# Optimization experiments

Hardware: AMD Instinct MI355X
Metric: run time of the kernel (lower is better)

The kernel has to match this reference:

```python
import jax, jax.numpy as jnp
import numpy as np

N = 100000
IN_DIM = 256
OUT_DIM = 256
E = 3200000
SLOPE = 0.2


def setup_inputs() -> dict:
    key = jax.random.key(0)
    ks = jax.random.split(key, 14)
    xav = lambda k, shape: jax.random.normal(k, shape, jnp.float32) * np.sqrt(2.0 / sum(shape))
    inp = {
        "H": jax.random.normal(ks[0], (N, IN_DIM), jnp.float32),
        "W0": xav(ks[1], (IN_DIM, OUT_DIM)),
        "W1": xav(ks[2], (IN_DIM, OUT_DIM)),
        "W2": xav(ks[3], (IN_DIM, OUT_DIM)),
        "a0": xav(ks[4], (2 * OUT_DIM,)),
        "a1": xav(ks[5], (2 * OUT_DIM,)),
        "a2": xav(ks[6], (2 * OUT_DIM,)),
        "bias": jnp.zeros((OUT_DIM,), jnp.float32),
    }
    for i, r in enumerate(["0", "1", "2"]):
        inp["row" + r] = jax.random.randint(ks[7 + 2 * i], (E,), 0, N, jnp.int32)
        inp["col" + r] = jax.random.randint(ks[8 + 2 * i], (E,), 0, N, jnp.int32)
    return inp


def _gat_type(H, W, a, row, col):
    # Wh: [N, out_dim]
    Wh = H @ W
    # attention logits per edge: leaky_relu(a_dst . Wh[row] + a_src . Wh[col])
    s_dst = Wh @ a[:OUT_DIM]   # [N]
    s_src = Wh @ a[OUT_DIM:]   # [N]
    e = jax.nn.leaky_relu(s_dst[row] + s_src[col], SLOPE)  # [E]
    # segment softmax over destination node (row)
    e_max = jax.ops.segment_max(e, row, num_segments=N)    # [N]
    e_shifted = jnp.exp(e - e_max[row])
    e_sum = jax.ops.segment_sum(e_shifted, row, num_segments=N)
    alpha = e_shifted / jnp.maximum(e_sum[row], 1e-12)     # [E]
    # weighted aggregation of source features into destinations
    return jax.ops.segment_sum(alpha[:, None] * Wh[col], row, num_segments=N)


def reference(H, row0, col0, row1, col1, row2, col2, W0, W1, W2, a0, a1, a2, bias):
    out = _gat_type(H, W0, a0, row0, col0)
    out = out + _gat_type(H, W1, a1, row1, col1)
    out = out + _gat_type(H, W2, a2, row2, col2)
    return out + bias
```

## Files before the change

kernel.cpp:

```cpp
#include <hip/hip_runtime.h>
#include <cstdint>
#include <cstddef>

#define DIM 256
#define SLOPE 0.2f
#define BSHIFT 8
#define SLOTS 9216
#define TILE 4096

typedef __attribute__((ext_vector_type(8))) short short8;
typedef __attribute__((ext_vector_type(4))) float f32x4;

__device__ __forceinline__ unsigned short f2bf(float f) {
  unsigned u = __float_as_uint(f);
  u += 0x7fffu + ((u >> 16) & 1u);
  return (unsigned short)(u >> 16);
}
__device__ __forceinline__ float bf2f(unsigned short h) {
  return __uint_as_float(((unsigned)h) << 16);
}

__global__ void wtrans_kernel(const float* __restrict__ W0, const float* __restrict__ W1,
                              const float* __restrict__ W2, unsigned short* __restrict__ Wt) {
  const float* W = blockIdx.y == 0 ? W0 : (blockIdx.y == 1 ? W1 : W2);
  int k = blockIdx.x, n = threadIdx.x;
  Wt[((size_t)blockIdx.y * DIM + n) * DIM + k] = f2bf(W[k * DIM + n]);
}

__global__ __launch_bounds__(256, 2) void gemm_scores_kernel(
    const float* __restrict__ H, const unsigned short* __restrict__ Wt,
    const float* __restrict__ a, unsigned short* __restrict__ Whb,
    float* __restrict__ s_dst, float* __restrict__ s_src, int N) {
  __shared__ unsigned short Hs[64][264];
  __shared__ unsigned short Os[4][16][264];
  const int t = threadIdx.x;
  const int r0 = blockIdx.x * 64;
#pragma unroll
  for (int i = 0; i < 16; ++i) {
    int idx = t + i * 256;
    int row = idx >> 6;
    int c4 = idx & 63;
    int r = r0 + row;
    float4 h = (r < N) ? *(const float4*)&H[(size_t)r * DIM + c4 * 4]
                       : make_float4(0.f, 0.f, 0.f, 0.f);
    unsigned lo = (unsigned)f2bf(h.x) | ((unsigned)f2bf(h.y) << 16);
    unsigned hi = (unsigned)f2bf(h.z) | ((unsigned)f2bf(h.w) << 16);
    *(uint2*)&Hs[row][c4 * 4] = make_uint2(lo, hi);
  }
  __syncthreads();
  const int wave = t >> 6, lane = t & 63;
  const int q = lane >> 4, m = lane & 15;
  const int rowbase = wave * 16;
  short8 Af[8];
#pragma unroll
  for (int k0 = 0; k0 < 8; ++k0)
    Af[k0] = *(const short8*)&Hs[rowbase + m][k0 * 32 + q * 8];
  f32x4 acc[16];
#pragma unroll
  for (int j = 0; j < 16; ++j) acc[j] = (f32x4){0.f, 0.f, 0.f, 0.f};
#pragma unroll
  for (int k0 = 0; k0 < 8; ++k0) {
#pragma unroll
    for (int j = 0; j < 16; ++j) {
      short8 Bf = *(const short8*)&Wt[(size_t)(j * 16 + m) * DIM + k0 * 32 + q * 8];
      acc[j] = __builtin_amdgcn_mfma_f32_16x16x32_bf16(Af[k0], Bf, acc[j], 0, 0, 0);
    }
  }
  float pd[4] = {0, 0, 0, 0}, ps[4] = {0, 0, 0, 0};
#pragma unroll
  for (int j = 0; j < 16; ++j) {
    int col = j * 16 + m;
    float ad = a[col], as = a[DIM + col];
#pragma unroll
    for (int reg = 0; reg < 4; ++reg) {
      float v = acc[j][reg];
      pd[reg] += v * ad;
      ps[reg] += v * as;
      Os[wave][q * 4 + reg][col] = f2bf(v);
    }
  }
#pragma unroll
  for (int off = 8; off >= 1; off >>= 1) {
#pragma unroll
    for (int reg = 0; reg < 4; ++reg) {
      pd[reg] += __shfl_down(pd[reg], off);
      ps[reg] += __shfl_down(ps[reg], off);
    }
  }
  if (m == 0) {
#pragma unroll
    for (int reg = 0; reg < 4; ++reg) {
      int r = r0 + rowbase + q * 4 + reg;
      if (r < N) {
        s_dst[r] = pd[reg];
        s_src[r] = ps[reg];
      }
    }
  }
  __syncthreads();
#pragma unroll
  for (int row = 0; row < 16; ++row) {
    int r = r0 + rowbase + row;
    if (r < N)
      *(uint2*)&Whb[(size_t)r * DIM + lane * 4] = *(const uint2*)&Os[wave][row][lane * 4];
  }
}

__global__ __launch_bounds__(256) void bin_edges_kernel(
    const int* __restrict__ r0, const int* __restrict__ r1, const int* __restrict__ r2,
    const int* __restrict__ c0, const int* __restrict__ c1, const int* __restrict__ c2,
    int* __restrict__ bcnt,
    unsigned* __restrict__ pairs,
    int E, int NB) {
  __shared__ int hist[512];
  __shared__ int curs[512];
  const int ty = blockIdx.y;
  const int* rr = ty == 0 ? r0 : (ty == 1 ? r1 : r2);
  const int* cc = ty == 0 ? c0 : (ty == 1 ? c1 : c2);
  const int t = threadIdx.x;
  const int base = blockIdx.x * TILE;
  for (int i = t; i < NB; i += 256) hist[i] = 0;
  __syncthreads();
  int rows[TILE / 256];
#pragma unroll
  for (int i = 0; i < TILE / 256; ++i) {
    int e = base + t + i * 256;
    int r = (e < E) ? rr[e] : -1;
    rows[i] = r;
    if (r >= 0) atomicAdd(&hist[r >> BSHIFT], 1);
  }
  __syncthreads();
  for (int b = t; b < NB; b += 256) {
    int h = hist[b];
    int off = h ? atomicAdd(&bcnt[ty * NB + b], h) : 0;
    curs[b] = b * SLOTS + off;
  }
  __syncthreads();
  unsigned* pt = pairs + (size_t)ty * NB * SLOTS;
#pragma unroll
  for (int i = 0; i < TILE / 256; ++i) {
    int e = base + t + i * 256;
    if (e >= E) continue;
    int r = rows[i];
    int b = r >> BSHIFT;
    int pos = atomicAdd(&curs[b], 1);
    if (pos - b * SLOTS < SLOTS)
      pt[pos] = ((unsigned)(r & 255) << 17) | (unsigned)cc[e];
  }
}

__global__ __launch_bounds__(256) void bucket_sort_kernel(
    const int* __restrict__ bcnt, unsigned* __restrict__ pairs,
    int* __restrict__ rp, int* __restrict__ deg, int N, int NB) {
  __shared__ int hist[256];
  __shared__ int excl[256];
  __shared__ int curs[256];
  __shared__ unsigned stage[SLOTS];
  const int b = blockIdx.x, ty = blockIdx.y;
  const int t = threadIdx.x;
  int cnt = bcnt[ty * NB + b];
  if (cnt > SLOTS) cnt = SLOTS;
  unsigned* pb = pairs + (size_t)ty * NB * SLOTS + (size_t)b * SLOTS;
  hist[t] = 0;
  __syncthreads();
  for (int i = t; i < cnt; i += 256) atomicAdd(&hist[pb[i] >> 17], 1);
  __syncthreads();
  int v = hist[t];
  excl[t] = v;
  __syncthreads();
  for (int off = 1; off < 256; off <<= 1) {
    int u = (t >= off) ? excl[t - off] : 0;
    __syncthreads();
    excl[t] += u;
    __syncthreads();
  }
  int ex = excl[t] - v;
  curs[t] = ex;
  int r = (b << BSHIFT) + t;
  if (r < N) {
    rp[(size_t)ty * N + r] = b * SLOTS + ex;
    deg[(size_t)ty * N + r] = v;
  }
  __syncthreads();
  for (int i = t; i < cnt; i += 256) {
    unsigned p = pb[i];
    int pos = atomicAdd(&curs[p >> 17], 1);
    stage[pos] = p;
  }
  __syncthreads();
  for (int i = t; i < cnt; i += 256) pb[i] = stage[i];
}

__global__ __launch_bounds__(256) void gat_node_kernel(
    const int* __restrict__ rp, const int* __restrict__ deg,
    const unsigned* __restrict__ pcol,
    const float* __restrict__ s_dst, const float* __restrict__ s_src,
    const unsigned short* __restrict__ Whb,
    const float* __restrict__ bias, float* __restrict__ out, int N, int first) {
  __shared__ uint2 ebuf[4][64];
  int n = (int)((blockIdx.x * (unsigned)blockDim.x + threadIdx.x) >> 6);
  if (n >= N) return;
  const int wid = (threadIdx.x >> 6);
  const int lane = threadIdx.x & 63;
  int beg = rp[n], d = deg[n], end = beg + d;
  if (!first && d == 0) return;
  float sd = s_dst[n];
  float mx = -__builtin_inff();
  for (int p = beg + lane; p < end; p += 64) {
    float v = sd + s_src[pcol[p] & 0x1FFFFu];
    v = v > 0.f ? v : SLOPE * v;
    mx = fmaxf(mx, v);
  }
#pragma unroll
  for (int off = 32; off >= 1; off >>= 1) mx = fmaxf(mx, __shfl_down(mx, off));
  mx = __shfl(mx, 0);
  const unsigned short* wbase = Whb + lane * 4;
  float4 acc = {0.f, 0.f, 0.f, 0.f};
  float psum = 0.f;
  for (int base = beg; base < end; base += 64) {
    int myp = base + lane;
    int cnt = end - base;
    if (cnt > 64) cnt = 64;
    unsigned myc = 0;
    float mype = 0.f;
    if (myp < end) {
      myc = pcol[myp] & 0x1FFFFu;
      float v = sd + s_src[myc];
      v = v > 0.f ? v : SLOPE * v;
      mype = __expf(v - mx);
    }
    psum += mype;
    ebuf[wid][lane] = make_uint2(myc, __float_as_uint(mype));
#pragma unroll 4
    for (int j = 0; j < cnt; ++j) {
      uint2 cp = ebuf[wid][j];
      float pe = __uint_as_float(cp.y);
      ushort4 w = *(const ushort4*)&wbase[(size_t)cp.x * DIM];
      acc.x += pe * bf2f(w.x);
      acc.y += pe * bf2f(w.y);
      acc.z += pe * bf2f(w.z);
      acc.w += pe * bf2f(w.w);
    }
  }
#pragma unroll
  for (int off = 32; off >= 1; off >>= 1) psum += __shfl_down(psum, off);
  psum = __shfl(psum, 0);
  float inv = 1.f / fmaxf(psum, 1e-12f);
  float4* o = (float4*)(out + (size_t)n * DIM) + lane;
  float4 cur = first ? ((const float4*)bias)[lane] : *o;
  cur.x += acc.x * inv;
  cur.y += acc.y * inv;
  cur.z += acc.z * inv;
  cur.w += acc.w * inv;
  *o = cur;
}

static inline size_t align256(size_t x) { return (x + 255) & ~(size_t)255; }

extern "C" void kernel_launch(void* const* d_in, const int* in_sizes, int n_in,
                              void* d_out, int out_size, void* d_ws, size_t ws_size,
                              hipStream_t stream) {
  const float* H = (const float*)d_in[0];
  const float* W[3] = {(const float*)d_in[1], (const float*)d_in[2], (const float*)d_in[3]};
  const float* a[3] = {(const float*)d_in[4], (const float*)d_in[5], (const float*)d_in[6]};
  const float* bias = (const float*)d_in[7];
  const int* row[3] = {(const int*)d_in[8], (const int*)d_in[10], (const int*)d_in[12]};
  const int* col[3] = {(const int*)d_in[9], (const int*)d_in[11], (const int*)d_in[13]};
  const int N = in_sizes[0] / DIM;
  const int E = in_sizes[8];
  const int NB = (N + 255) >> BSHIFT;
  float* out = (float*)d_out;

  char* ws = (char*)d_ws;
  size_t off = 0;
  unsigned short* Whb = (unsigned short*)(ws + off);
  off = align256(off + (size_t)N * DIM * sizeof(unsigned short));
  unsigned short* Wt = (unsigned short*)(ws + off);
  off = align256(off + (size_t)3 * DIM * DIM * sizeof(unsigned short));
  float* s_dst = (float*)(ws + off);
  off = align256(off + (size_t)N * sizeof(float));
  float* s_src = (float*)(ws + off);
  off = align256(off + (size_t)N * sizeof(float));
  int* bcnt = (int*)(ws + off);
  off = align256(off + (size_t)3 * NB * sizeof(int));
  int* rp = (int*)(ws + off);
  off = align256(off + (size_t)3 * N * sizeof(int));
  int* deg = (int*)(ws + off);
  off = align256(off + (size_t)3 * N * sizeof(int));
  unsigned* pairs = (unsigned*)(ws + off);
  off = align256(off + (size_t)3 * NB * SLOTS * sizeof(unsigned));

  wtrans_kernel<<<dim3(DIM, 3), 256, 0, stream>>>(W[0], W[1], W[2], Wt);
  hipMemsetAsync(bcnt, 0, (size_t)3 * NB * sizeof(int), stream);
  const int eb = (E + TILE - 1) / TILE;
  bin_edges_kernel<<<dim3(eb, 3), 256, 0, stream>>>(row[0], row[1], row[2], col[0], col[1],
                                                    col[2], bcnt, pairs, E, NB);
  bucket_sort_kernel<<<dim3(NB, 3), 256, 0, stream>>>(bcnt, pairs, rp, deg, N, NB);

  for (int t = 0; t < 3; ++t) {
    gemm_scores_kernel<<<(N + 63) / 64, 256, 0, stream>>>(H, Wt + (size_t)t * DIM * DIM, a[t],
                                                          Whb, s_dst, s_src, N);
    gat_node_kernel<<<(N * 64 + 255) / 256, 256, 0, stream>>>(
        rp + (size_t)t * N, deg + (size_t)t * N, pairs + (size_t)t * NB * SLOTS, s_dst, s_src,
        Whb, bias, out, N, t == 0 ? 1 : 0);
  }
  (void)n_in;
  (void)out_size;
  (void)ws_size;
}
```

Before: 1.546 ms.

## Replace per-node softmax max pass with global score bound; shrink GEMM LDS

```diff
diff --git a/kernel.cpp b/kernel.cpp
--- a/kernel.cpp
+++ b/kernel.cpp
@@ -27,12 +27,12 @@
   Wt[((size_t)blockIdx.y * DIM + n) * DIM + k] = f2bf(W[k * DIM + n]);
 }
 
-__global__ __launch_bounds__(256, 2) void gemm_scores_kernel(
+__global__ __launch_bounds__(256, 3) void gemm_scores_kernel(
     const float* __restrict__ H, const unsigned short* __restrict__ Wt,
     const float* __restrict__ a, unsigned short* __restrict__ Whb,
-    float* __restrict__ s_dst, float* __restrict__ s_src, int N) {
+    float* __restrict__ s_dst, float* __restrict__ s_src,
+    unsigned* __restrict__ smax_u, int N) {
   __shared__ unsigned short Hs[64][264];
-  __shared__ unsigned short Os[4][16][264];
   const int t = threadIdx.x;
   const int r0 = blockIdx.x * 64;
 #pragma unroll
@@ -66,6 +66,7 @@
       acc[j] = __builtin_amdgcn_mfma_f32_16x16x32_bf16(Af[k0], Bf, acc[j], 0, 0, 0);
     }
   }
+  unsigned short(*Os)[264] = &Hs[rowbase];
   float pd[4] = {0, 0, 0, 0}, ps[4] = {0, 0, 0, 0};
 #pragma unroll
   for (int j = 0; j < 16; ++j) {
@@ -76,7 +77,7 @@
       float v = acc[j][reg];
       pd[reg] += v * ad;
       ps[reg] += v * as;
-      Os[wave][q * 4 + reg][col] = f2bf(v);
+      Os[q * 4 + reg][col] = f2bf(v);
     }
   }
 #pragma unroll
@@ -88,6 +89,10 @@
     }
   }
   if (m == 0) {
+    float lmax = fmaxf(fmaxf(ps[0], ps[1]), fmaxf(ps[2], ps[3]));
+    int ib = __float_as_int(lmax);
+    unsigned key = (unsigned)ib ^ ((unsigned)(ib >> 31) | 0x80000000u);
+    atomicMax(smax_u, key);
 #pragma unroll
     for (int reg = 0; reg < 4; ++reg) {
       int r = r0 + rowbase + q * 4 + reg;
@@ -97,12 +102,11 @@
       }
     }
   }
-  __syncthreads();
 #pragma unroll
   for (int row = 0; row < 16; ++row) {
     int r = r0 + rowbase + row;
     if (r < N)
-      *(uint2*)&Whb[(size_t)r * DIM + lane * 4] = *(const uint2*)&Os[wave][row][lane * 4];
+      *(uint2*)&Whb[(size_t)r * DIM + lane * 4] = *(const uint2*)&Os[row][lane * 4];
   }
 }
 
@@ -195,6 +199,7 @@
     const int* __restrict__ rp, const int* __restrict__ deg,
     const unsigned* __restrict__ pcol,
     const float* __restrict__ s_dst, const float* __restrict__ s_src,
+    const unsigned* __restrict__ smax_u,
     const unsigned short* __restrict__ Whb,
     const float* __restrict__ bias, float* __restrict__ out, int N, int first) {
   __shared__ uint2 ebuf[4][64];
@@ -204,16 +209,11 @@
   const int lane = threadIdx.x & 63;
   int beg = rp[n], d = deg[n], end = beg + d;
   if (!first && d == 0) return;
+  unsigned u = *smax_u;
+  float smax = (u & 0x80000000u) ? __uint_as_float(u ^ 0x80000000u)
+                                 : __uint_as_float(~u);
   float sd = s_dst[n];
-  float mx = -__builtin_inff();
-  for (int p = beg + lane; p < end; p += 64) {
-    float v = sd + s_src[pcol[p] & 0x1FFFFu];
-    v = v > 0.f ? v : SLOPE * v;
-    mx = fmaxf(mx, v);
-  }
-#pragma unroll
-  for (int off = 32; off >= 1; off >>= 1) mx = fmaxf(mx, __shfl_down(mx, off));
-  mx = __shfl(mx, 0);
+  float mx = sd + smax;
   const unsigned short* wbase = Whb + lane * 4;
   float4 acc = {0.f, 0.f, 0.f, 0.f};
   float psum = 0.f;
@@ -231,7 +231,7 @@
     }
     psum += mype;
     ebuf[wid][lane] = make_uint2(myc, __float_as_uint(mype));
-#pragma unroll 4
+#pragma unroll 8
     for (int j = 0; j < cnt; ++j) {
       uint2 cp = ebuf[wid][j];
       float pe = __uint_as_float(cp.y);
@@ -283,6 +283,8 @@
   off = align256(off + (size_t)N * sizeof(float));
   int* bcnt = (int*)(ws + off);
   off = align256(off + (size_t)3 * NB * sizeof(int));
+  unsigned* smax = (unsigned*)(ws + off);
+  off = align256(off + 256);
   int* rp = (int*)(ws + off);
   off = align256(off + (size_t)3 * N * sizeof(int));
   int* deg = (int*)(ws + off);
@@ -292,6 +294,7 @@
 
   wtrans_kernel<<<dim3(DIM, 3), 256, 0, stream>>>(W[0], W[1], W[2], Wt);
   hipMemsetAsync(bcnt, 0, (size_t)3 * NB * sizeof(int), stream);
+  hipMemsetAsync(smax, 0, 3 * sizeof(unsigned), stream);
   const int eb = (E + TILE - 1) / TILE;
   bin_edges_kernel<<<dim3(eb, 3), 256, 0, stream>>>(row[0], row[1], row[2], col[0], col[1],
                                                     col[2], bcnt, pairs, E, NB);
@@ -299,10 +302,10 @@
 
   for (int t = 0; t < 3; ++t) {
     gemm_scores_kernel<<<(N + 63) / 64, 256, 0, stream>>>(H, Wt + (size_t)t * DIM * DIM, a[t],
-                                                          Whb, s_dst, s_src, N);
+                                                          Whb, s_dst, s_src, smax + t, N);
     gat_node_kernel<<<(N * 64 + 255) / 256, 256, 0, stream>>>(
         rp + (size_t)t * N, deg + (size_t)t * N, pairs + (size_t)t * NB * SLOTS, s_dst, s_src,
-        Whb, bias, out, N, t == 0 ? 1 : 0);
+        smax + t, Whb, bias, out, N, t == 0 ? 1 : 0);
   }
   (void)n_in;
   (void)out_size;
```

Result: slower. 1.691 ms (+9.3%).

## Fuse three per-type GAT aggregations into one kernel accumulating in registers

Applied to the files above, without the earlier changes.

```diff
diff --git a/kernel.cpp b/kernel.cpp
--- a/kernel.cpp
+++ b/kernel.cpp
@@ -189,6 +189,80 @@
   }
   __syncthreads();
   for (int i = t; i < cnt; i += 256) pb[i] = stage[i];
+}
+
+__global__ __launch_bounds__(256) void gat_fused_kernel(
+    const int* __restrict__ rp, const int* __restrict__ deg,
+    const unsigned* __restrict__ pairs,
+    const float* __restrict__ s_dst, const float* __restrict__ s_src,
+    const unsigned short* __restrict__ Whb,
+    const float* __restrict__ bias, float* __restrict__ out, int N, int NB) {
+  __shared__ uint2 ebuf[4][64];
+  int n = (int)((blockIdx.x * (unsigned)blockDim.x + threadIdx.x) >> 6);
+  if (n >= N) return;
+  const int wid = (threadIdx.x >> 6);
+  const int lane = threadIdx.x & 63;
+  const size_t NDIM = (size_t)N * DIM;
+  float4 total = {0.f, 0.f, 0.f, 0.f};
+  for (int t = 0; t < 3; ++t) {
+    int beg = rp[(size_t)t * N + n], d = deg[(size_t)t * N + n];
+    if (d == 0) continue;
+    int end = beg + d;
+    const unsigned* pcol = pairs + (size_t)t * NB * SLOTS;
+    const float* ss = s_src + (size_t)t * N;
+    float sd = s_dst[(size_t)t * N + n];
+    const unsigned short* wbase = Whb + (size_t)t * NDIM + lane * 4;
+    float mx = -__builtin_inff();
+    for (int p = beg + lane; p < end; p += 64) {
+      float v = sd + ss[pcol[p] & 0x1FFFFu];
+      v = v > 0.f ? v : SLOPE * v;
+      mx = fmaxf(mx, v);
+    }
+#pragma unroll
+    for (int off = 32; off >= 1; off >>= 1) mx = fmaxf(mx, __shfl_down(mx, off));
+    mx = __shfl(mx, 0);
+    float4 acc = {0.f, 0.f, 0.f, 0.f};
+    float psum = 0.f;
+    for (int base = beg; base < end; base += 64) {
+      int myp = base + lane;
+      int cnt = end - base;
+      if (cnt > 64) cnt = 64;
+      unsigned myc = 0;
+      float mype = 0.f;
+      if (myp < end) {
+        myc = pcol[myp] & 0x1FFFFu;
+        float v = sd + ss[myc];
+        v = v > 0.f ? v : SLOPE * v;
+        mype = __expf(v - mx);
+      }
+      psum += mype;
+      ebuf[wid][lane] = make_uint2(myc, __float_as_uint(mype));
+#pragma unroll 8
+      for (int j = 0; j < cnt; ++j) {
+        uint2 cp = ebuf[wid][j];
+        float pe = __uint_as_float(cp.y);
+        ushort4 w = *(const ushort4*)&wbase[(size_t)cp.x * DIM];
+        acc.x += pe * bf2f(w.x);
+        acc.y += pe * bf2f(w.y);
+        acc.z += pe * bf2f(w.z);
+        acc.w += pe * bf2f(w.w);
+      }
+    }
+#pragma unroll
+    for (int off = 32; off >= 1; off >>= 1) psum += __shfl_down(psum, off);
+    psum = __shfl(psum, 0);
+    float inv = 1.f / fmaxf(psum, 1e-12f);
+    total.x += acc.x * inv;
+    total.y += acc.y * inv;
+    total.z += acc.z * inv;
+    total.w += acc.w * inv;
+  }
+  float4 cur = ((const float4*)bias)[lane];
+  cur.x += total.x;
+  cur.y += total.y;
+  cur.z += total.z;
+  cur.w += total.w;
+  *((float4*)(out + (size_t)n * DIM) + lane) = cur;
 }
 
 __global__ __launch_bounds__(256) void gat_node_kernel(
@@ -231,7 +305,7 @@
     }
     psum += mype;
     ebuf[wid][lane] = make_uint2(myc, __float_as_uint(mype));
-#pragma unroll 4
+#pragma unroll 8
     for (int j = 0; j < cnt; ++j) {
       uint2 cp = ebuf[wid][j];
       float pe = __uint_as_float(cp.y);
@@ -273,14 +347,12 @@
 
   char* ws = (char*)d_ws;
   size_t off = 0;
-  unsigned short* Whb = (unsigned short*)(ws + off);
-  off = align256(off + (size_t)N * DIM * sizeof(unsigned short));
   unsigned short* Wt = (unsigned short*)(ws + off);
   off = align256(off + (size_t)3 * DIM * DIM * sizeof(unsigned short));
   float* s_dst = (float*)(ws + off);
-  off = align256(off + (size_t)N * sizeof(float));
+  off = align256(off + (size_t)3 * N * sizeof(float));
   float* s_src = (float*)(ws + off);
-  off = align256(off + (size_t)N * sizeof(float));
+  off = align256(off + (size_t)3 * N * sizeof(float));
   int* bcnt = (int*)(ws + off);
   off = align256(off + (size_t)3 * NB * sizeof(int));
   int* rp = (int*)(ws + off);
@@ -289,6 +361,9 @@
   off = align256(off + (size_t)3 * N * sizeof(int));
   unsigned* pairs = (unsigned*)(ws + off);
   off = align256(off + (size_t)3 * NB * SLOTS * sizeof(unsigned));
+  unsigned short* Whb = (unsigned short*)(ws + off);
+  const size_t whb_bytes = align256((size_t)N * DIM * sizeof(unsigned short));
+  const int fused = (ws_size >= off + 3 * whb_bytes) ? 1 : 0;
 
   wtrans_kernel<<<dim3(DIM, 3), 256, 0, stream>>>(W[0], W[1], W[2], Wt);
   hipMemsetAsync(bcnt, 0, (size_t)3 * NB * sizeof(int), stream);
@@ -297,12 +372,25 @@
                                                     col[2], bcnt, pairs, E, NB);
   bucket_sort_kernel<<<dim3(NB, 3), 256, 0, stream>>>(bcnt, pairs, rp, deg, N, NB);
 
-  for (int t = 0; t < 3; ++t) {
-    gemm_scores_kernel<<<(N + 63) / 64, 256, 0, stream>>>(H, Wt + (size_t)t * DIM * DIM, a[t],
-                                                          Whb, s_dst, s_src, N);
-    gat_node_kernel<<<(N * 64 + 255) / 256, 256, 0, stream>>>(
-        rp + (size_t)t * N, deg + (size_t)t * N, pairs + (size_t)t * NB * SLOTS, s_dst, s_src,
-        Whb, bias, out, N, t == 0 ? 1 : 0);
+  const int gemm_blocks = (N + 63) / 64;
+  const int gat_blocks = (N * 64 + 255) / 256;
+  if (fused) {
+    for (int t = 0; t < 3; ++t)
+      gemm_scores_kernel<<<gemm_blocks, 256, 0, stream>>>(
+          H, Wt + (size_t)t * DIM * DIM, a[t],
+          Whb + t * (whb_bytes / sizeof(unsigned short)),
+          s_dst + (size_t)t * N, s_src + (size_t)t * N, N);
+    gat_fused_kernel<<<gat_blocks, 256, 0, stream>>>(rp, deg, pairs, s_dst, s_src, Whb, bias,
+                                                     out, N, NB);
+  } else {
+    for (int t = 0; t < 3; ++t) {
+      gemm_scores_kernel<<<gemm_blocks, 256, 0, stream>>>(H, Wt + (size_t)t * DIM * DIM, a[t],
+                                                          Whb, s_dst + (size_t)t * N,
+                                                          s_src + (size_t)t * N, N);
+      gat_node_kernel<<<gat_blocks, 256, 0, stream>>>(
+          rp + (size_t)t * N, deg + (size_t)t * N, pairs + (size_t)t * NB * SLOTS,
+          s_dst + (size_t)t * N, s_src + (size_t)t * N, Whb, bias, out, N, t == 0 ? 1 : 0);
+    }
   }
   (void)n_in;
   (void)out_size;
```

New measurement: 1.533 ms. No clear change (-0.9%).
